# Kernel tuning notes

Measured on AMD Instinct MI355X. Metric: run time of the kernel, lower is better.

## Reference

```python
import jax, jax.numpy as jnp
import numpy as np

N = 50000      # nodes
E = 800000     # directed edges (before self-loops)
IN_DIM = 128
HID = 64
HEADS = 4
OUT_DIM = 64
NEG_SLOPE = 0.2


def setup_inputs() -> dict:
    key = jax.random.key(0)
    ks = jax.random.split(key, 14)
    glorot = lambda k, shape: jax.random.normal(k, shape, jnp.float32) * np.sqrt(2.0 / (shape[0] + shape[-1]))
    return {
        "x": jax.random.normal(ks[0], (N, IN_DIM), jnp.float32),
        "edge_index": jax.random.randint(ks[1], (2, E), 0, N, jnp.int64),
        "edge_attr": jax.random.normal(ks[2], (E, 16), jnp.float32),  # ignored (GATConv has edge_dim=None)
        # gat1: IN_DIM -> HEADS*HID
        "W1": glorot(ks[3], (IN_DIM, HEADS * HID)),
        "a_src1": glorot(ks[4], (HEADS, HID)),
        "a_dst1": glorot(ks[5], (HEADS, HID)),
        "b1": jnp.zeros((HEADS * HID,), jnp.float32),
        # gat2: HEADS*HID -> HEADS*HID
        "W2": glorot(ks[6], (HEADS * HID, HEADS * HID)),
        "a_src2": glorot(ks[7], (HEADS, HID)),
        "a_dst2": glorot(ks[8], (HEADS, HID)),
        "b2": jnp.zeros((HEADS * HID,), jnp.float32),
        # fc head
        "Wfc": glorot(ks[9], (HEADS * HID, OUT_DIM)),
        "bfc": jnp.zeros((OUT_DIM,), jnp.float32),
    }


def _gat_conv(x, src, dst, W, a_src, a_dst, b, num_nodes):
    """PyG GATConv, concat=True, add_self_loops handled by caller."""
    H, C = a_src.shape
    xh = (x @ W).reshape(-1, H, C)                         # [N, H, C]
    alpha_src = jnp.einsum('nhc,hc->nh', xh, a_src)        # [N, H]
    alpha_dst = jnp.einsum('nhc,hc->nh', xh, a_dst)
    e = jax.nn.leaky_relu(alpha_src[src] + alpha_dst[dst], NEG_SLOPE)  # [Etot, H]
    # segment softmax over incoming edges of each dst node
    m = jax.ops.segment_max(e, dst, num_segments=num_nodes)
    a = jnp.exp(e - jax.lax.stop_gradient(m)[dst])
    denom = jax.ops.segment_sum(a, dst, num_segments=num_nodes)
    alpha = a / (denom[dst] + 1e-16)                        # [Etot, H]
    msg = xh[src] * alpha[:, :, None]                       # gather + weight  [Etot, H, C]
    out = jax.ops.segment_sum(msg, dst, num_segments=num_nodes)  # scatter-agg [N, H, C]
    return out.reshape(num_nodes, H * C) + b


def reference(x, edge_index, edge_attr, W1, a_src1, a_dst1, b1,
              W2, a_src2, a_dst2, b2, Wfc, bfc):
    num_nodes = x.shape[0]
    loop = jnp.arange(num_nodes, dtype=edge_index.dtype)
    src = jnp.concatenate([edge_index[0], loop])  # add_self_loops=True (PyG default)
    dst = jnp.concatenate([edge_index[1], loop])
    h = jax.nn.relu(_gat_conv(x, src, dst, W1, a_src1, a_dst1, b1, num_nodes))
    h = jax.nn.relu(_gat_conv(h, src, dst, W2, a_src2, a_dst2, b2, num_nodes))
    return h @ Wfc + bfc
```

## Files before the change

### kernel.cpp

```cpp
#include <hip/hip_runtime.h>
#include <hip/hip_bf16.h>

#define N_NODES 50000
#define E_EDGES 800000
#define ETOT (E_EDGES + N_NODES)
#define IN_DIM 128
#define HID 64
#define HEADS 4
#define HC (HEADS * HID)
#define OUT_DIM 64
#define NEG_SLOPE 0.2f
#define SCAN_BLK 1024

using bf16x8 = __attribute__((ext_vector_type(8))) __bf16;
using f32x4  = __attribute__((ext_vector_type(4))) float;

__global__ __launch_bounds__(256) void cvt_bf16(const float* __restrict__ in,
                                                __hip_bfloat16* __restrict__ out,
                                                long n4) {
    long i = (long)blockIdx.x * 256 + threadIdx.x;
    if (i >= n4) return;
    float4 v = ((const float4*)in)[i];
    __hip_bfloat162 a, b;
    a.x = __float2bfloat16(v.x); a.y = __float2bfloat16(v.y);
    b.x = __float2bfloat16(v.z); b.y = __float2bfloat16(v.w);
    ((__hip_bfloat162*)out)[2 * i]     = a;
    ((__hip_bfloat162*)out)[2 * i + 1] = b;
}

__global__ __launch_bounds__(256) void prep_weights(const float* __restrict__ W1,
                                                    const float* __restrict__ W2,
                                                    const float* __restrict__ Wfc,
                                                    __hip_bfloat16* __restrict__ W1t,
                                                    __hip_bfloat16* __restrict__ W2t,
                                                    __hip_bfloat16* __restrict__ Wft) {
    int i = blockIdx.x * 256 + threadIdx.x;
    if (i < 32768) {
        int k = i >> 8, n = i & 255;
        W1t[n * IN_DIM + k] = __float2bfloat16(W1[i]);
    } else if (i < 98304) {
        int j = i - 32768;
        int k = j >> 8, n = j & 255;
        W2t[n * HC + k] = __float2bfloat16(W2[j]);
    } else if (i < 114688) {
        int j = i - 98304;
        int k = j >> 6, n = j & 63;
        Wft[n * HC + k] = __float2bfloat16(Wfc[j]);
    }
}

template <int K>
__global__ __launch_bounds__(256) void gemm_xh_mfma(const __hip_bfloat16* __restrict__ A,
                                                    const __hip_bfloat16* __restrict__ Bt,
                                                    __hip_bfloat16* __restrict__ Cb,
                                                    int M,
                                                    const float* __restrict__ a_src,
                                                    const float* __restrict__ a_dst,
                                                    float* __restrict__ as_,
                                                    float* __restrict__ ad_) {
    constexpr int LDSA = 64 * (K + 8) * 2;
    constexpr int LDSC = 64 * HC * 2;
    constexpr int SMEM = LDSA > LDSC ? LDSA : LDSC;
    __shared__ char smem[SMEM];
    unsigned short (*Atile)[K + 8] = (unsigned short (*)[K + 8])smem;

    const int t = threadIdx.x;
    const int h = t >> 6;
    const int lane = t & 63;
    const int l15 = lane & 15, l4 = lane >> 4;
    const int m0 = blockIdx.x * 64;

    constexpr int KB8 = K / 8;
#pragma unroll
    for (int i = 0; i < K / 32; i++) {
        int q = i * 256 + t;
        int row = q / KB8;
        int kc = (q - row * KB8) * 8;
        int gm = m0 + row;
        uint4 v = make_uint4(0, 0, 0, 0);
        if (gm < M) v = *(const uint4*)(A + (long)gm * K + kc);
        *(uint4*)&Atile[row][kc] = v;
    }
    __syncthreads();

    f32x4 acc[4][4];
#pragma unroll
    for (int i = 0; i < 4; i++)
#pragma unroll
        for (int j = 0; j < 4; j++) acc[i][j] = (f32x4)0.f;

    const __hip_bfloat16* Bp = Bt + ((long)(h * 64 + l15)) * K + l4 * 8;
    constexpr int NK = K / 32;
    bf16x8 bcur[4], bnxt[4];
#pragma unroll
    for (int cb = 0; cb < 4; cb++) bcur[cb] = *(const bf16x8*)(Bp + (long)cb * 16 * K);

#pragma unroll
    for (int kb = 0; kb < NK; kb++) {
        if (kb + 1 < NK) {
#pragma unroll
            for (int cb = 0; cb < 4; cb++)
                bnxt[cb] = *(const bf16x8*)(Bp + (long)cb * 16 * K + (kb + 1) * 32);
        }
        bf16x8 afr[4];
#pragma unroll
        for (int rb = 0; rb < 4; rb++)
            afr[rb] = *(const bf16x8*)&Atile[rb * 16 + l15][kb * 32 + l4 * 8];
#pragma unroll
        for (int rb = 0; rb < 4; rb++)
#pragma unroll
            for (int cb = 0; cb < 4; cb++)
                acc[rb][cb] = __builtin_amdgcn_mfma_f32_16x16x32_bf16(afr[rb], bcur[cb], acc[rb][cb], 0, 0, 0);
#pragma unroll
        for (int cb = 0; cb < 4; cb++) bcur[cb] = bnxt[cb];
    }

    float asv[4], adv[4];
#pragma unroll
    for (int cb = 0; cb < 4; cb++) {
        asv[cb] = a_src[h * HID + cb * 16 + l15];
        adv[cb] = a_dst[h * HID + cb * 16 + l15];
    }
#pragma unroll
    for (int rb = 0; rb < 4; rb++) {
#pragma unroll
        for (int reg = 0; reg < 4; reg++) {
            int row = m0 + rb * 16 + l4 * 4 + reg;
            float ps = 0.f, pd = 0.f;
#pragma unroll
            for (int cb = 0; cb < 4; cb++) {
                ps += acc[rb][cb][reg] * asv[cb];
                pd += acc[rb][cb][reg] * adv[cb];
            }
#pragma unroll
            for (int off = 8; off; off >>= 1) {
                ps += __shfl_down(ps, off);
                pd += __shfl_down(pd, off);
            }
            if (l15 == 0 && row < M) {
                as_[row * HEADS + h] = ps;
                ad_[row * HEADS + h] = pd;
            }
        }
    }

    __syncthreads();
    unsigned short* Ct = (unsigned short*)smem;
#pragma unroll
    for (int rb = 0; rb < 4; rb++) {
#pragma unroll
        for (int cb = 0; cb < 4; cb++) {
#pragma unroll
            for (int reg = 0; reg < 4; reg++) {
                int rl = rb * 16 + l4 * 4 + reg;
                int col = h * 64 + cb * 16 + l15;
                __hip_bfloat16 bv = __float2bfloat16(acc[rb][cb][reg]);
                Ct[rl * HC + col] = *(unsigned short*)&bv;
            }
        }
    }
    __syncthreads();
#pragma unroll
    for (int i = 0; i < 8; i++) {
        int idx = i * 256 + t;
        int row = idx >> 5;
        int cc  = idx & 31;
        int gm = m0 + row;
        if (gm < M)
            *(uint4*)&Cb[(long)gm * HC + cc * 8] = *(const uint4*)&Ct[row * HC + cc * 8];
    }
}

__global__ __launch_bounds__(256) void gemm_fc_mfma(const __hip_bfloat16* __restrict__ A,
                                                    const __hip_bfloat16* __restrict__ Bt,
                                                    const float* __restrict__ bias,
                                                    float* __restrict__ C,
                                                    int M) {
    constexpr int K = 256;
    constexpr int LDSA = 64 * (K + 8) * 2;
    __shared__ char smem[LDSA];
    unsigned short (*Atile)[K + 8] = (unsigned short (*)[K + 8])smem;

    const int t = threadIdx.x;
    const int w = t >> 6;
    const int lane = t & 63;
    const int l15 = lane & 15, l4 = lane >> 4;
    const int m0 = blockIdx.x * 64;

    constexpr int KB8 = K / 8;
#pragma unroll
    for (int i = 0; i < K / 32; i++) {
        int q = i * 256 + t;
        int row = q / KB8;
        int kc = (q - row * KB8) * 8;
        int gm = m0 + row;
        uint4 v = make_uint4(0, 0, 0, 0);
        if (gm < M) v = *(const uint4*)(A + (long)gm * K + kc);
        *(uint4*)&Atile[row][kc] = v;
    }
    __syncthreads();

    f32x4 acc[4];
#pragma unroll
    for (int j = 0; j < 4; j++) acc[j] = (f32x4)0.f;

    const __hip_bfloat16* Bp = Bt + (long)l15 * K + l4 * 8;
#pragma unroll
    for (int kb = 0; kb < K / 32; kb++) {
        bf16x8 afr = *(const bf16x8*)&Atile[w * 16 + l15][kb * 32 + l4 * 8];
#pragma unroll
        for (int cb = 0; cb < 4; cb++) {
            bf16x8 bfr = *(const bf16x8*)(Bp + (long)cb * 16 * K + kb * 32);
            acc[cb] = __builtin_amdgcn_mfma_f32_16x16x32_bf16(afr, bfr, acc[cb], 0, 0, 0);
        }
    }

    __syncthreads();
    float* Ct = (float*)smem;
#pragma unroll
    for (int cb = 0; cb < 4; cb++) {
        int col = cb * 16 + l15;
        float bv = bias[col];
#pragma unroll
        for (int reg = 0; reg < 4; reg++) {
            int rl = w * 16 + l4 * 4 + reg;
            Ct[rl * OUT_DIM + col] = acc[cb][reg] + bv;
        }
    }
    __syncthreads();
#pragma unroll
    for (int i = 0; i < 4; i++) {
        int idx = i * 256 + t;
        int row = idx >> 4;
        int cc  = idx & 15;
        int gm = m0 + row;
        if (gm < M)
            *(uint4*)&C[(long)gm * OUT_DIM + cc * 4] = *(const uint4*)&Ct[row * OUT_DIM + cc * 4];
    }
}

__global__ __launch_bounds__(256) void hist_kernel(const int* __restrict__ ei,
                                                   int* __restrict__ deg) {
    int e = blockIdx.x * 256 + threadIdx.x;
    if (e >= ETOT) return;
    int d = (e < E_EDGES) ? ei[E_EDGES + e] : e - E_EDGES;
    atomicAdd(&deg[d], 1);
}

__global__ __launch_bounds__(SCAN_BLK) void scan_phase1(const int* __restrict__ deg,
                                                        int* __restrict__ rs,
                                                        int* __restrict__ partials,
                                                        int n) {
    __shared__ int tmp[SCAN_BLK];
    int i = blockIdx.x * SCAN_BLK + threadIdx.x;
    int v = (i < n) ? deg[i] : 0;
    tmp[threadIdx.x] = v;
    __syncthreads();
    for (int off = 1; off < SCAN_BLK; off <<= 1) {
        int t = (threadIdx.x >= (unsigned)off) ? tmp[threadIdx.x - off] : 0;
        __syncthreads();
        tmp[threadIdx.x] += t;
        __syncthreads();
    }
    if (i < n) rs[i] = tmp[threadIdx.x];
    if (threadIdx.x == SCAN_BLK - 1) partials[blockIdx.x] = tmp[SCAN_BLK - 1];
}

__global__ __launch_bounds__(SCAN_BLK) void scan_phase3(const int* __restrict__ deg,
                                                        int* __restrict__ rs,
                                                        int* __restrict__ cursor,
                                                        const int* __restrict__ partials,
                                                        int nb, int n) {
    __shared__ int sOff[2];
    if (threadIdx.x < 64) {
        int lane = threadIdx.x;
        int v = (lane < nb) ? partials[lane] : 0;
#pragma unroll
        for (int off = 1; off < 64; off <<= 1) {
            int tv = __shfl_up(v, off);
            if (lane >= off) v += tv;
        }
        if ((int)blockIdx.x > 0 && lane == (int)blockIdx.x - 1) sOff[0] = v;
        if (lane == nb - 1) sOff[1] = v;
        if (blockIdx.x == 0 && lane == 0) sOff[0] = 0;
    }
    __syncthreads();
    int i = blockIdx.x * SCAN_BLK + threadIdx.x;
    if (i < n) {
        int e = rs[i] + sOff[0] - deg[i];
        rs[i] = e;
        cursor[i] = e;
    } else if (i == n) {
        rs[n] = sOff[1];
    }
}

__global__ __launch_bounds__(256) void fill_kernel(const int* __restrict__ ei,
                                                   int* __restrict__ cursor,
                                                   int* __restrict__ csr_src) {
    int e = blockIdx.x * 256 + threadIdx.x;
    if (e >= ETOT) return;
    int s, d;
    if (e < E_EDGES) { s = ei[e]; d = ei[E_EDGES + e]; }
    else             { s = d = e - E_EDGES; }
    int pos = atomicAdd(&cursor[d], 1);
    csr_src[pos] = s;
}

__global__ __launch_bounds__(256) void agg_kernel(const int* __restrict__ rs,
                                                  const int* __restrict__ csr_src,
                                                  const __hip_bfloat16* __restrict__ xh,
                                                  const float* __restrict__ as_,
                                                  const float* __restrict__ ad_,
                                                  const float* __restrict__ bias,
                                                  __hip_bfloat16* __restrict__ out) {
    int wid = threadIdx.x >> 6;
    int n = blockIdx.x * 4 + wid;
    if (n >= N_NODES) return;
    int lane = threadIdx.x & 63;
    int h = lane >> 4;
    int cq = lane;
    int beg = rs[n], end = rs[n + 1];
    float adv = ad_[n * HEADS + h];
    float acc0 = 0.f, acc1 = 0.f, acc2 = 0.f, acc3 = 0.f, wsum = 0.f;
    const uint2* xh4 = (const uint2*)xh;
#pragma unroll 4
    for (int p = beg; p < end; ++p) {
        int s = csr_src[p];
        float l = as_[s * HEADS + h] + adv;
        l = l > 0.f ? l : NEG_SLOPE * l;
        float wv = __expf(l);
        wsum += wv;
        uint2 v = xh4[(long)s * (HC / 4) + cq];
        float f0 = __uint_as_float(v.x << 16);
        float f1 = __uint_as_float(v.x & 0xffff0000u);
        float f2 = __uint_as_float(v.y << 16);
        float f3 = __uint_as_float(v.y & 0xffff0000u);
        acc0 += wv * f0;
        acc1 += wv * f1;
        acc2 += wv * f2;
        acc3 += wv * f3;
    }
    float inv = 1.f / (wsum + 1e-16f);
    float4 bi = *(const float4*)&bias[4 * lane];
    __hip_bfloat162 p01, p23;
    p01.x = __float2bfloat16(fmaxf(acc0 * inv + bi.x, 0.f));
    p01.y = __float2bfloat16(fmaxf(acc1 * inv + bi.y, 0.f));
    p23.x = __float2bfloat16(fmaxf(acc2 * inv + bi.z, 0.f));
    p23.y = __float2bfloat16(fmaxf(acc3 * inv + bi.w, 0.f));
    uint2 pk;
    pk.x = *(unsigned int*)&p01;
    pk.y = *(unsigned int*)&p23;
    *(uint2*)&out[(long)n * HC + 4 * lane] = pk;
}

extern "C" void kernel_launch(void* const* d_in, const int* in_sizes, int n_in,
                              void* d_out, int out_size, void* d_ws, size_t ws_size,
                              hipStream_t stream) {
    const float* x    = (const float*)d_in[0];
    const int*   ei   = (const int*)d_in[1];
    const float* W1   = (const float*)d_in[3];
    const float* a_s1 = (const float*)d_in[4];
    const float* a_d1 = (const float*)d_in[5];
    const float* b1   = (const float*)d_in[6];
    const float* W2   = (const float*)d_in[7];
    const float* a_s2 = (const float*)d_in[8];
    const float* a_d2 = (const float*)d_in[9];
    const float* b2   = (const float*)d_in[10];
    const float* Wfc  = (const float*)d_in[11];
    const float* bfc  = (const float*)d_in[12];
    float* out = (float*)d_out;

    char* ws = (char*)d_ws;
    size_t off = 0;
    __hip_bfloat16* xb  = (__hip_bfloat16*)(ws + off); off += (size_t)N_NODES * IN_DIM * 2;
    __hip_bfloat16* xh  = (__hip_bfloat16*)(ws + off); off += (size_t)N_NODES * HC * 2;
    __hip_bfloat16* y   = (__hip_bfloat16*)(ws + off); off += (size_t)N_NODES * HC * 2;
    __hip_bfloat16* W1t = (__hip_bfloat16*)(ws + off); off += (size_t)HC * IN_DIM * 2;
    __hip_bfloat16* W2t = (__hip_bfloat16*)(ws + off); off += (size_t)HC * HC * 2;
    __hip_bfloat16* Wft = (__hip_bfloat16*)(ws + off); off += (size_t)OUT_DIM * HC * 2;
    float* asb     = (float*)(ws + off); off += (size_t)N_NODES * HEADS * 4;
    float* adb     = (float*)(ws + off); off += (size_t)N_NODES * HEADS * 4;
    int*   deg     = (int*)(ws + off);   off += (size_t)N_NODES * 4;
    int*   rs      = (int*)(ws + off);   off += (size_t)(N_NODES + 1) * 4;
    int*   cursor  = (int*)(ws + off);   off += (size_t)N_NODES * 4;
    int*   partials= (int*)(ws + off);   off += 256 * 4;
    int*   csr_src = (int*)(ws + off);   off += (size_t)ETOT * 4;

    int mblocks = (N_NODES + 63) / 64;
    int edge_blocks  = (ETOT + 255) / 256;
    int scan_blocks  = (N_NODES + SCAN_BLK - 1) / SCAN_BLK;
    int scan_blocks3 = (N_NODES + 1 + SCAN_BLK - 1) / SCAN_BLK;
    int agg_blocks   = (N_NODES + 3) / 4;

    long x4 = (long)N_NODES * IN_DIM / 4;
    cvt_bf16<<<(int)((x4 + 255) / 256), 256, 0, stream>>>(x, xb, x4);
    prep_weights<<<(114688 + 255) / 256, 256, 0, stream>>>(W1, W2, Wfc, W1t, W2t, Wft);

    hipMemsetAsync(deg, 0, (size_t)N_NODES * 4, stream);
    hist_kernel<<<edge_blocks, 256, 0, stream>>>(ei, deg);
    scan_phase1<<<scan_blocks, SCAN_BLK, 0, stream>>>(deg, rs, partials, N_NODES);
    scan_phase3<<<scan_blocks3, SCAN_BLK, 0, stream>>>(deg, rs, cursor, partials, scan_blocks, N_NODES);
    fill_kernel<<<edge_blocks, 256, 0, stream>>>(ei, cursor, csr_src);

    gemm_xh_mfma<IN_DIM><<<mblocks, 256, 0, stream>>>(xb, W1t, xh, N_NODES, a_s1, a_d1, asb, adb);
    agg_kernel<<<agg_blocks, 256, 0, stream>>>(rs, csr_src, xh, asb, adb, b1, y);

    gemm_xh_mfma<HC><<<mblocks, 256, 0, stream>>>(y, W2t, xh, N_NODES, a_s2, a_d2, asb, adb);
    agg_kernel<<<agg_blocks, 256, 0, stream>>>(rs, csr_src, xh, asb, adb, b2, y);

    gemm_fc_mfma<<<mblocks, 256, 0, stream>>>(y, Wft, bfc, out, N_NODES);
}
```

Before: 421.5 us.

## Fuse prologue kernels, single-block scan, split aggregation launches, unroll more

Merges the input bf16 conversion, the weight transpose/convert and the degree histogram into one prologue kernel with block-range dispatch. Replaces the two-phase multi-block scan with a single 1024-thread block that scans 49 elements per thread. Splits each aggregation launch into two half-node launches and raises the edge-loop unroll from 4 to 8. The aim is fewer kernel launches and less inter-kernel overhead, at the cost of a serial single-block scan and an extra launch per aggregation layer.

Measured after the change: 549.7 us. 1.3x slower.

```diff
diff --git a/kernel.cpp b/kernel.cpp
--- a/kernel.cpp
+++ b/kernel.cpp
@@ -10,43 +10,97 @@
 #define HC (HEADS * HID)
 #define OUT_DIM 64
 #define NEG_SLOPE 0.2f
-#define SCAN_BLK 1024
 
 using bf16x8 = __attribute__((ext_vector_type(8))) __bf16;
 using f32x4  = __attribute__((ext_vector_type(4))) float;
 
-__global__ __launch_bounds__(256) void cvt_bf16(const float* __restrict__ in,
-                                                __hip_bfloat16* __restrict__ out,
-                                                long n4) {
-    long i = (long)blockIdx.x * 256 + threadIdx.x;
-    if (i >= n4) return;
-    float4 v = ((const float4*)in)[i];
-    __hip_bfloat162 a, b;
-    a.x = __float2bfloat16(v.x); a.y = __float2bfloat16(v.y);
-    b.x = __float2bfloat16(v.z); b.y = __float2bfloat16(v.w);
-    ((__hip_bfloat162*)out)[2 * i]     = a;
-    ((__hip_bfloat162*)out)[2 * i + 1] = b;
-}
-
-__global__ __launch_bounds__(256) void prep_weights(const float* __restrict__ W1,
-                                                    const float* __restrict__ W2,
-                                                    const float* __restrict__ Wfc,
-                                                    __hip_bfloat16* __restrict__ W1t,
-                                                    __hip_bfloat16* __restrict__ W2t,
-                                                    __hip_bfloat16* __restrict__ Wft) {
-    int i = blockIdx.x * 256 + threadIdx.x;
-    if (i < 32768) {
-        int k = i >> 8, n = i & 255;
-        W1t[n * IN_DIM + k] = __float2bfloat16(W1[i]);
-    } else if (i < 98304) {
-        int j = i - 32768;
-        int k = j >> 8, n = j & 255;
-        W2t[n * HC + k] = __float2bfloat16(W2[j]);
-    } else if (i < 114688) {
-        int j = i - 98304;
-        int k = j >> 6, n = j & 63;
-        Wft[n * HC + k] = __float2bfloat16(Wfc[j]);
-    }
+#define CVT_BLOCKS 6250
+#define PREP_BLOCKS 448
+#define HIST_BLOCKS 3321
+__global__ __launch_bounds__(256) void prologue_kernel(const float* __restrict__ x,
+                                                       __hip_bfloat16* __restrict__ xb,
+                                                       const float* __restrict__ W1,
+                                                       const float* __restrict__ W2,
+                                                       const float* __restrict__ Wfc,
+                                                       __hip_bfloat16* __restrict__ W1t,
+                                                       __hip_bfloat16* __restrict__ W2t,
+                                                       __hip_bfloat16* __restrict__ Wft,
+                                                       const int* __restrict__ ei,
+                                                       int* __restrict__ deg) {
+    int b = blockIdx.x;
+    if (b < CVT_BLOCKS) {
+        long i = (long)b * 256 + threadIdx.x;
+        float4 v = ((const float4*)x)[i];
+        __hip_bfloat162 a2, b2;
+        a2.x = __float2bfloat16(v.x); a2.y = __float2bfloat16(v.y);
+        b2.x = __float2bfloat16(v.z); b2.y = __float2bfloat16(v.w);
+        ((__hip_bfloat162*)xb)[2 * i]     = a2;
+        ((__hip_bfloat162*)xb)[2 * i + 1] = b2;
+    } else if (b < CVT_BLOCKS + PREP_BLOCKS) {
+        int i = (b - CVT_BLOCKS) * 256 + threadIdx.x;
+        if (i < 32768) {
+            int k = i >> 8, n = i & 255;
+            W1t[n * IN_DIM + k] = __float2bfloat16(W1[i]);
+        } else if (i < 98304) {
+            int j = i - 32768;
+            int k = j >> 8, n = j & 255;
+            W2t[n * HC + k] = __float2bfloat16(W2[j]);
+        } else if (i < 114688) {
+            int j = i - 98304;
+            int k = j >> 6, n = j & 63;
+            Wft[n * HC + k] = __float2bfloat16(Wfc[j]);
+        }
+    } else {
+        int e = (b - CVT_BLOCKS - PREP_BLOCKS) * 256 + threadIdx.x;
+        if (e >= ETOT) return;
+        int d = (e < E_EDGES) ? ei[E_EDGES + e] : e - E_EDGES;
+        atomicAdd(&deg[d], 1);
+    }
+}
+
+__global__ __launch_bounds__(1024) void scan_all(const int* __restrict__ deg,
+                                                 int* __restrict__ rs,
+                                                 int* __restrict__ cursor,
+                                                 int n) {
+    __shared__ int tot[1024];
+    const int t = threadIdx.x;
+    const int base = t * 49;
+    int s = 0;
+    for (int j = 0; j < 49; j++) {
+        int i = base + j;
+        if (i < n) s += deg[i];
+    }
+    tot[t] = s;
+    __syncthreads();
+    for (int off = 1; off < 1024; off <<= 1) {
+        int v = (t >= off) ? tot[t - off] : 0;
+        __syncthreads();
+        tot[t] += v;
+        __syncthreads();
+    }
+    int run = (t == 0) ? 0 : tot[t - 1];
+    for (int j = 0; j < 49; j++) {
+        int i = base + j;
+        if (i < n) {
+            int d = deg[i];
+            rs[i] = run;
+            cursor[i] = run;
+            run += d;
+        }
+    }
+    if (t == 1023) rs[n] = tot[1023];
+}
+
+__global__ __launch_bounds__(256) void fill_kernel(const int* __restrict__ ei,
+                                                   int* __restrict__ cursor,
+                                                   int* __restrict__ csr_src) {
+    int e = blockIdx.x * 256 + threadIdx.x;
+    if (e >= ETOT) return;
+    int s, d;
+    if (e < E_EDGES) { s = ei[e]; d = ei[E_EDGES + e]; }
+    else             { s = d = e - E_EDGES; }
+    int pos = atomicAdd(&cursor[d], 1);
+    csr_src[pos] = s;
 }
 
 template <int K>
@@ -239,83 +293,16 @@
     }
 }
 
-__global__ __launch_bounds__(256) void hist_kernel(const int* __restrict__ ei,
-                                                   int* __restrict__ deg) {
-    int e = blockIdx.x * 256 + threadIdx.x;
-    if (e >= ETOT) return;
-    int d = (e < E_EDGES) ? ei[E_EDGES + e] : e - E_EDGES;
-    atomicAdd(&deg[d], 1);
-}
-
-__global__ __launch_bounds__(SCAN_BLK) void scan_phase1(const int* __restrict__ deg,
-                                                        int* __restrict__ rs,
-                                                        int* __restrict__ partials,
-                                                        int n) {
-    __shared__ int tmp[SCAN_BLK];
-    int i = blockIdx.x * SCAN_BLK + threadIdx.x;
-    int v = (i < n) ? deg[i] : 0;
-    tmp[threadIdx.x] = v;
-    __syncthreads();
-    for (int off = 1; off < SCAN_BLK; off <<= 1) {
-        int t = (threadIdx.x >= (unsigned)off) ? tmp[threadIdx.x - off] : 0;
-        __syncthreads();
-        tmp[threadIdx.x] += t;
-        __syncthreads();
-    }
-    if (i < n) rs[i] = tmp[threadIdx.x];
-    if (threadIdx.x == SCAN_BLK - 1) partials[blockIdx.x] = tmp[SCAN_BLK - 1];
-}
-
-__global__ __launch_bounds__(SCAN_BLK) void scan_phase3(const int* __restrict__ deg,
-                                                        int* __restrict__ rs,
-                                                        int* __restrict__ cursor,
-                                                        const int* __restrict__ partials,
-                                                        int nb, int n) {
-    __shared__ int sOff[2];
-    if (threadIdx.x < 64) {
-        int lane = threadIdx.x;
-        int v = (lane < nb) ? partials[lane] : 0;
-#pragma unroll
-        for (int off = 1; off < 64; off <<= 1) {
-            int tv = __shfl_up(v, off);
-            if (lane >= off) v += tv;
-        }
-        if ((int)blockIdx.x > 0 && lane == (int)blockIdx.x - 1) sOff[0] = v;
-        if (lane == nb - 1) sOff[1] = v;
-        if (blockIdx.x == 0 && lane == 0) sOff[0] = 0;
-    }
-    __syncthreads();
-    int i = blockIdx.x * SCAN_BLK + threadIdx.x;
-    if (i < n) {
-        int e = rs[i] + sOff[0] - deg[i];
-        rs[i] = e;
-        cursor[i] = e;
-    } else if (i == n) {
-        rs[n] = sOff[1];
-    }
-}
-
-__global__ __launch_bounds__(256) void fill_kernel(const int* __restrict__ ei,
-                                                   int* __restrict__ cursor,
-                                                   int* __restrict__ csr_src) {
-    int e = blockIdx.x * 256 + threadIdx.x;
-    if (e >= ETOT) return;
-    int s, d;
-    if (e < E_EDGES) { s = ei[e]; d = ei[E_EDGES + e]; }
-    else             { s = d = e - E_EDGES; }
-    int pos = atomicAdd(&cursor[d], 1);
-    csr_src[pos] = s;
-}
-
 __global__ __launch_bounds__(256) void agg_kernel(const int* __restrict__ rs,
                                                   const int* __restrict__ csr_src,
                                                   const __hip_bfloat16* __restrict__ xh,
                                                   const float* __restrict__ as_,
                                                   const float* __restrict__ ad_,
                                                   const float* __restrict__ bias,
-                                                  __hip_bfloat16* __restrict__ out) {
+                                                  __hip_bfloat16* __restrict__ out,
+                                                  int base) {
     int wid = threadIdx.x >> 6;
-    int n = blockIdx.x * 4 + wid;
+    int n = base + blockIdx.x * 4 + wid;
     if (n >= N_NODES) return;
     int lane = threadIdx.x & 63;
     int h = lane >> 4;
@@ -324,7 +311,7 @@
     float adv = ad_[n * HEADS + h];
     float acc0 = 0.f, acc1 = 0.f, acc2 = 0.f, acc3 = 0.f, wsum = 0.f;
     const uint2* xh4 = (const uint2*)xh;
-#pragma unroll 4
+#pragma unroll 8
     for (int p = beg; p < end; ++p) {
         int s = csr_src[p];
         float l = as_[s * HEADS + h] + adv;
@@ -384,30 +371,26 @@
     int*   deg     = (int*)(ws + off);   off += (size_t)N_NODES * 4;
     int*   rs      = (int*)(ws + off);   off += (size_t)(N_NODES + 1) * 4;
     int*   cursor  = (int*)(ws + off);   off += (size_t)N_NODES * 4;
-    int*   partials= (int*)(ws + off);   off += 256 * 4;
     int*   csr_src = (int*)(ws + off);   off += (size_t)ETOT * 4;
 
     int mblocks = (N_NODES + 63) / 64;
-    int edge_blocks  = (ETOT + 255) / 256;
-    int scan_blocks  = (N_NODES + SCAN_BLK - 1) / SCAN_BLK;
-    int scan_blocks3 = (N_NODES + 1 + SCAN_BLK - 1) / SCAN_BLK;
-    int agg_blocks   = (N_NODES + 3) / 4;
-
-    long x4 = (long)N_NODES * IN_DIM / 4;
-    cvt_bf16<<<(int)((x4 + 255) / 256), 256, 0, stream>>>(x, xb, x4);
-    prep_weights<<<(114688 + 255) / 256, 256, 0, stream>>>(W1, W2, Wfc, W1t, W2t, Wft);
+    int edge_blocks = (ETOT + 255) / 256;
+    int half_blocks = 6250;
 
     hipMemsetAsync(deg, 0, (size_t)N_NODES * 4, stream);
-    hist_kernel<<<edge_blocks, 256, 0, stream>>>(ei, deg);
-    scan_phase1<<<scan_blocks, SCAN_BLK, 0, stream>>>(deg, rs, partials, N_NODES);
-    scan_phase3<<<scan_blocks3, SCAN_BLK, 0, stream>>>(deg, rs, cursor, partials, scan_blocks, N_NODES);
+    prologue_kernel<<<CVT_BLOCKS + PREP_BLOCKS + HIST_BLOCKS, 256, 0, stream>>>(
+        x, xb, W1, W2, Wfc, W1t, W2t, Wft, ei, deg);
+
+    scan_all<<<1, 1024, 0, stream>>>(deg, rs, cursor, N_NODES);
     fill_kernel<<<edge_blocks, 256, 0, stream>>>(ei, cursor, csr_src);
 
     gemm_xh_mfma<IN_DIM><<<mblocks, 256, 0, stream>>>(xb, W1t, xh, N_NODES, a_s1, a_d1, asb, adb);
-    agg_kernel<<<agg_blocks, 256, 0, stream>>>(rs, csr_src, xh, asb, adb, b1, y);
+    agg_kernel<<<half_blocks, 256, 0, stream>>>(rs, csr_src, xh, asb, adb, b1, y, 0);
+    agg_kernel<<<half_blocks, 256, 0, stream>>>(rs, csr_src, xh, asb, adb, b1, y, 25000);
 
     gemm_xh_mfma<HC><<<mblocks, 256, 0, stream>>>(y, W2t, xh, N_NODES, a_s2, a_d2, asb, adb);
-    agg_kernel<<<agg_blocks, 256, 0, stream>>>(rs, csr_src, xh, asb, adb, b2, y);
+    agg_kernel<<<half_blocks, 256, 0, stream>>>(rs, csr_src, xh, asb, adb, b2, y, 0);
+    agg_kernel<<<half_blocks, 256, 0, stream>>>(rs, csr_src, xh, asb, adb, b2, y, 25000);
 
     gemm_fc_mfma<<<mblocks, 256, 0, stream>>>(y, Wft, bfc, out, N_NODES);
 }
```

## Merge prologue kernels into one launch and split aggregation into halves

Applied to the files above, without the earlier changes.

The bf16 conversion of x, the weight transpose/convert and the degree histogram are folded into one kernel that picks its role from the block index, cutting two launches. Each aggregation is now launched as two half-node launches of 6250 blocks each, and the edge loop unroll goes from 4 to 8. The split adds launches back and serialises the halves, so it may cost time. The larger unroll can raise register pressure.

New measurement: 429.7 us. Within noise of the previous version (+1.9%).

```diff
diff --git a/kernel.cpp b/kernel.cpp
--- a/kernel.cpp
+++ b/kernel.cpp
@@ -15,38 +15,108 @@
 using bf16x8 = __attribute__((ext_vector_type(8))) __bf16;
 using f32x4  = __attribute__((ext_vector_type(4))) float;
 
-__global__ __launch_bounds__(256) void cvt_bf16(const float* __restrict__ in,
-                                                __hip_bfloat16* __restrict__ out,
-                                                long n4) {
-    long i = (long)blockIdx.x * 256 + threadIdx.x;
-    if (i >= n4) return;
-    float4 v = ((const float4*)in)[i];
-    __hip_bfloat162 a, b;
-    a.x = __float2bfloat16(v.x); a.y = __float2bfloat16(v.y);
-    b.x = __float2bfloat16(v.z); b.y = __float2bfloat16(v.w);
-    ((__hip_bfloat162*)out)[2 * i]     = a;
-    ((__hip_bfloat162*)out)[2 * i + 1] = b;
-}
-
-__global__ __launch_bounds__(256) void prep_weights(const float* __restrict__ W1,
-                                                    const float* __restrict__ W2,
-                                                    const float* __restrict__ Wfc,
-                                                    __hip_bfloat16* __restrict__ W1t,
-                                                    __hip_bfloat16* __restrict__ W2t,
-                                                    __hip_bfloat16* __restrict__ Wft) {
-    int i = blockIdx.x * 256 + threadIdx.x;
-    if (i < 32768) {
-        int k = i >> 8, n = i & 255;
-        W1t[n * IN_DIM + k] = __float2bfloat16(W1[i]);
-    } else if (i < 98304) {
-        int j = i - 32768;
-        int k = j >> 8, n = j & 255;
-        W2t[n * HC + k] = __float2bfloat16(W2[j]);
-    } else if (i < 114688) {
-        int j = i - 98304;
-        int k = j >> 6, n = j & 63;
-        Wft[n * HC + k] = __float2bfloat16(Wfc[j]);
-    }
+#define CVT_BLOCKS 6250
+#define PREP_BLOCKS 448
+#define HIST_BLOCKS 3321
+__global__ __launch_bounds__(256) void prologue_kernel(const float* __restrict__ x,
+                                                       __hip_bfloat16* __restrict__ xb,
+                                                       const float* __restrict__ W1,
+                                                       const float* __restrict__ W2,
+                                                       const float* __restrict__ Wfc,
+                                                       __hip_bfloat16* __restrict__ W1t,
+                                                       __hip_bfloat16* __restrict__ W2t,
+                                                       __hip_bfloat16* __restrict__ Wft,
+                                                       const int* __restrict__ ei,
+                                                       int* __restrict__ deg) {
+    int b = blockIdx.x;
+    if (b < CVT_BLOCKS) {
+        long i = (long)b * 256 + threadIdx.x;
+        float4 v = ((const float4*)x)[i];
+        __hip_bfloat162 a2, b2;
+        a2.x = __float2bfloat16(v.x); a2.y = __float2bfloat16(v.y);
+        b2.x = __float2bfloat16(v.z); b2.y = __float2bfloat16(v.w);
+        ((__hip_bfloat162*)xb)[2 * i]     = a2;
+        ((__hip_bfloat162*)xb)[2 * i + 1] = b2;
+    } else if (b < CVT_BLOCKS + PREP_BLOCKS) {
+        int i = (b - CVT_BLOCKS) * 256 + threadIdx.x;
+        if (i < 32768) {
+            int k = i >> 8, n = i & 255;
+            W1t[n * IN_DIM + k] = __float2bfloat16(W1[i]);
+        } else if (i < 98304) {
+            int j = i - 32768;
+            int k = j >> 8, n = j & 255;
+            W2t[n * HC + k] = __float2bfloat16(W2[j]);
+        } else if (i < 114688) {
+            int j = i - 98304;
+            int k = j >> 6, n = j & 63;
+            Wft[n * HC + k] = __float2bfloat16(Wfc[j]);
+        }
+    } else {
+        int e = (b - CVT_BLOCKS - PREP_BLOCKS) * 256 + threadIdx.x;
+        if (e >= ETOT) return;
+        int d = (e < E_EDGES) ? ei[E_EDGES + e] : e - E_EDGES;
+        atomicAdd(&deg[d], 1);
+    }
+}
+
+__global__ __launch_bounds__(SCAN_BLK) void scan_phase1(const int* __restrict__ deg,
+                                                        int* __restrict__ rs,
+                                                        int* __restrict__ partials,
+                                                        int n) {
+    __shared__ int tmp[SCAN_BLK];
+    int i = blockIdx.x * SCAN_BLK + threadIdx.x;
+    int v = (i < n) ? deg[i] : 0;
+    tmp[threadIdx.x] = v;
+    __syncthreads();
+    for (int off = 1; off < SCAN_BLK; off <<= 1) {
+        int t = (threadIdx.x >= (unsigned)off) ? tmp[threadIdx.x - off] : 0;
+        __syncthreads();
+        tmp[threadIdx.x] += t;
+        __syncthreads();
+    }
+    if (i < n) rs[i] = tmp[threadIdx.x];
+    if (threadIdx.x == SCAN_BLK - 1) partials[blockIdx.x] = tmp[SCAN_BLK - 1];
+}
+
+__global__ __launch_bounds__(SCAN_BLK) void scan_phase3(const int* __restrict__ deg,
+                                                        int* __restrict__ rs,
+                                                        int* __restrict__ cursor,
+                                                        const int* __restrict__ partials,
+                                                        int nb, int n) {
+    __shared__ int sOff[2];
+    if (threadIdx.x < 64) {
+        int lane = threadIdx.x;
+        int v = (lane < nb) ? partials[lane] : 0;
+#pragma unroll
+        for (int off = 1; off < 64; off <<= 1) {
+            int tv = __shfl_up(v, off);
+            if (lane >= off) v += tv;
+        }
+        if ((int)blockIdx.x > 0 && lane == (int)blockIdx.x - 1) sOff[0] = v;
+        if (lane == nb - 1) sOff[1] = v;
+        if (blockIdx.x == 0 && lane == 0) sOff[0] = 0;
+    }
+    __syncthreads();
+    int i = blockIdx.x * SCAN_BLK + threadIdx.x;
+    if (i < n) {
+        int e = rs[i] + sOff[0] - deg[i];
+        rs[i] = e;
+        cursor[i] = e;
+    } else if (i == n) {
+        rs[n] = sOff[1];
+    }
+}
+
+__global__ __launch_bounds__(256) void fill_kernel(const int* __restrict__ ei,
+                                                   int* __restrict__ cursor,
+                                                   int* __restrict__ csr_src) {
+    int e = blockIdx.x * 256 + threadIdx.x;
+    if (e >= ETOT) return;
+    int s, d;
+    if (e < E_EDGES) { s = ei[e]; d = ei[E_EDGES + e]; }
+    else             { s = d = e - E_EDGES; }
+    int pos = atomicAdd(&cursor[d], 1);
+    csr_src[pos] = s;
 }
 
 template <int K>
@@ -239,83 +309,16 @@
     }
 }
 
-__global__ __launch_bounds__(256) void hist_kernel(const int* __restrict__ ei,
-                                                   int* __restrict__ deg) {
-    int e = blockIdx.x * 256 + threadIdx.x;
-    if (e >= ETOT) return;
-    int d = (e < E_EDGES) ? ei[E_EDGES + e] : e - E_EDGES;
-    atomicAdd(&deg[d], 1);
-}
-
-__global__ __launch_bounds__(SCAN_BLK) void scan_phase1(const int* __restrict__ deg,
-                                                        int* __restrict__ rs,
-                                                        int* __restrict__ partials,
-                                                        int n) {
-    __shared__ int tmp[SCAN_BLK];
-    int i = blockIdx.x * SCAN_BLK + threadIdx.x;
-    int v = (i < n) ? deg[i] : 0;
-    tmp[threadIdx.x] = v;
-    __syncthreads();
-    for (int off = 1; off < SCAN_BLK; off <<= 1) {
-        int t = (threadIdx.x >= (unsigned)off) ? tmp[threadIdx.x - off] : 0;
-        __syncthreads();
-        tmp[threadIdx.x] += t;
-        __syncthreads();
-    }
-    if (i < n) rs[i] = tmp[threadIdx.x];
-    if (threadIdx.x == SCAN_BLK - 1) partials[blockIdx.x] = tmp[SCAN_BLK - 1];
-}
-
-__global__ __launch_bounds__(SCAN_BLK) void scan_phase3(const int* __restrict__ deg,
-                                                        int* __restrict__ rs,
-                                                        int* __restrict__ cursor,
-                                                        const int* __restrict__ partials,
-                                                        int nb, int n) {
-    __shared__ int sOff[2];
-    if (threadIdx.x < 64) {
-        int lane = threadIdx.x;
-        int v = (lane < nb) ? partials[lane] : 0;
-#pragma unroll
-        for (int off = 1; off < 64; off <<= 1) {
-            int tv = __shfl_up(v, off);
-            if (lane >= off) v += tv;
-        }
-        if ((int)blockIdx.x > 0 && lane == (int)blockIdx.x - 1) sOff[0] = v;
-        if (lane == nb - 1) sOff[1] = v;
-        if (blockIdx.x == 0 && lane == 0) sOff[0] = 0;
-    }
-    __syncthreads();
-    int i = blockIdx.x * SCAN_BLK + threadIdx.x;
-    if (i < n) {
-        int e = rs[i] + sOff[0] - deg[i];
-        rs[i] = e;
-        cursor[i] = e;
-    } else if (i == n) {
-        rs[n] = sOff[1];
-    }
-}
-
-__global__ __launch_bounds__(256) void fill_kernel(const int* __restrict__ ei,
-                                                   int* __restrict__ cursor,
-                                                   int* __restrict__ csr_src) {
-    int e = blockIdx.x * 256 + threadIdx.x;
-    if (e >= ETOT) return;
-    int s, d;
-    if (e < E_EDGES) { s = ei[e]; d = ei[E_EDGES + e]; }
-    else             { s = d = e - E_EDGES; }
-    int pos = atomicAdd(&cursor[d], 1);
-    csr_src[pos] = s;
-}
-
 __global__ __launch_bounds__(256) void agg_kernel(const int* __restrict__ rs,
                                                   const int* __restrict__ csr_src,
                                                   const __hip_bfloat16* __restrict__ xh,
                                                   const float* __restrict__ as_,
                                                   const float* __restrict__ ad_,
                                                   const float* __restrict__ bias,
-                                                  __hip_bfloat16* __restrict__ out) {
+                                                  __hip_bfloat16* __restrict__ out,
+                                                  int base) {
     int wid = threadIdx.x >> 6;
-    int n = blockIdx.x * 4 + wid;
+    int n = base + blockIdx.x * 4 + wid;
     if (n >= N_NODES) return;
     int lane = threadIdx.x & 63;
     int h = lane >> 4;
@@ -324,7 +327,7 @@
     float adv = ad_[n * HEADS + h];
     float acc0 = 0.f, acc1 = 0.f, acc2 = 0.f, acc3 = 0.f, wsum = 0.f;
     const uint2* xh4 = (const uint2*)xh;
-#pragma unroll 4
+#pragma unroll 8
     for (int p = beg; p < end; ++p) {
         int s = csr_src[p];
         float l = as_[s * HEADS + h] + adv;
@@ -388,26 +391,26 @@
     int*   csr_src = (int*)(ws + off);   off += (size_t)ETOT * 4;
 
     int mblocks = (N_NODES + 63) / 64;
-    int edge_blocks  = (ETOT + 255) / 256;
+    int edge_blocks = (ETOT + 255) / 256;
     int scan_blocks  = (N_NODES + SCAN_BLK - 1) / SCAN_BLK;
     int scan_blocks3 = (N_NODES + 1 + SCAN_BLK - 1) / SCAN_BLK;
-    int agg_blocks   = (N_NODES + 3) / 4;
-
-    long x4 = (long)N_NODES * IN_DIM / 4;
-    cvt_bf16<<<(int)((x4 + 255) / 256), 256, 0, stream>>>(x, xb, x4);
-    prep_weights<<<(114688 + 255) / 256, 256, 0, stream>>>(W1, W2, Wfc, W1t, W2t, Wft);
+    int half_blocks = 6250;
 
     hipMemsetAsync(deg, 0, (size_t)N_NODES * 4, stream);
-    hist_kernel<<<edge_blocks, 256, 0, stream>>>(ei, deg);
+    prologue_kernel<<<CVT_BLOCKS + PREP_BLOCKS + HIST_BLOCKS, 256, 0, stream>>>(
+        x, xb, W1, W2, Wfc, W1t, W2t, Wft, ei, deg);
+
     scan_phase1<<<scan_blocks, SCAN_BLK, 0, stream>>>(deg, rs, partials, N_NODES);
     scan_phase3<<<scan_blocks3, SCAN_BLK, 0, stream>>>(deg, rs, cursor, partials, scan_blocks, N_NODES);
     fill_kernel<<<edge_blocks, 256, 0, stream>>>(ei, cursor, csr_src);
 
     gemm_xh_mfma<IN_DIM><<<mblocks, 256, 0, stream>>>(xb, W1t, xh, N_NODES, a_s1, a_d1, asb, adb);
-    agg_kernel<<<agg_blocks, 256, 0, stream>>>(rs, csr_src, xh, asb, adb, b1, y);
+    agg_kernel<<<half_blocks, 256, 0, stream>>>(rs, csr_src, xh, asb, adb, b1, y, 0);
+    agg_kernel<<<half_blocks, 256, 0, stream>>>(rs, csr_src, xh, asb, adb, b1, y, 25000);
 
     gemm_xh_mfma<HC><<<mblocks, 256, 0, stream>>>(y, W2t, xh, N_NODES, a_s2, a_d2, asb, adb);
-    agg_kernel<<<agg_blocks, 256, 0, stream>>>(rs, csr_src, xh, asb, adb, b2, y);
+    agg_kernel<<<half_blocks, 256, 0, stream>>>(rs, csr_src, xh, asb, adb, b2, y, 0);
+    agg_kernel<<<half_blocks, 256, 0, stream>>>(rs, csr_src, xh, asb, adb, b2, y, 25000);
 
     gemm_fc_mfma<<<mblocks, 256, 0, stream>>>(y, Wft, bfc, out, N_NODES);
 }
```
